# Kernel optimization log

Hardware: AMD Instinct MI355X
Metric: run time of the kernel (lower is better)

Reference implementation:

```python
import jax, jax.numpy as jnp
import numpy as np

GAMMA = 0.99
GAE_LAMBDA = 0.95
SEQ_LEN = 1024
BATCH = 32768


def setup_inputs() -> dict:
    key = jax.random.key(0)
    k1, k2 = jax.random.split(key)
    rewards = jax.random.normal(k1, (SEQ_LEN, BATCH), dtype=jnp.float32)
    values = jax.random.normal(k2, (SEQ_LEN, BATCH), dtype=jnp.float32)
    return {"rewards": rewards, "values": values}


def _compute_advantages(rewards, values, gamma, gae_lambda):
    # delta_t = r_t + gamma * V_{t+1} - V_t  for t = 0 .. T-2  -> [T-1, B]
    deltas = rewards[:-1] + gamma * values[1:] - values[:-1]
    gl = gamma * gae_lambda

    def step(carry, delta):
        adv = delta + gl * carry
        return adv, adv

    init = jnp.zeros_like(deltas[0])
    # reverse scan implements the backward-in-time GAE recurrence
    _, advantages = jax.lax.scan(step, init, deltas, reverse=True)
    return advantages  # [T-1, B], equals torch advantages[:-1]


def reference(rewards, values):
    return _compute_advantages(rewards, values, GAMMA, GAE_LAMBDA)
```

## Files before the change

kernel.cpp:

```cpp
#include <hip/hip_runtime.h>
#include <math.h>


#define T_OUT 1023
#define B2    16384
#define NW    16
#define S_CH  64

#define GAMMA_F 0.99f
#define GL_F    0.9405f
#define INVG_F  1.0632642212653909f

typedef float f2v __attribute__((ext_vector_type(2)));

static __device__ __forceinline__ void nt_store_f2(float2* dst, float2 v) {
  __builtin_nontemporal_store(*(const f2v*)&v, (f2v*)dst);
}

#define STEP2(r, v)                                  \
  p.x = (r).x + GAMMA_F * vn.x - (v).x + GL_F * p.x; \
  p.y = (r).y + GAMMA_F * vn.y - (v).y + GL_F * p.y;

#define P1_LOADQ(rB_, vB_, tt)                       \
  _Pragma("unroll")                                  \
  for (int k = 0; k < 4; ++k) {                      \
    rB_[k] = rp[((tt) - k) * B2];                    \
    vB_[k] = vp[((tt) - k) * B2];                    \
  }

#define P1_COMPQ(rB_, vB_, tt)                       \
  _Pragma("unroll")                                  \
  for (int k = 0; k < 4; ++k) {                      \
    STEP2(rB_[k], vB_[k])                            \
    op[((tt) - k) * B2] = p;                         \
    vn = vB_[k];                                     \
  }

#define P1_BODY(rP, vP, rQ, vQ, rX, vX, rY, vY)      \
  P1_LOADQ(rP, vP, tp)                               \
  P1_LOADQ(rQ, vQ, tp - 4)                           \
  __builtin_amdgcn_sched_barrier(0);                 \
  P1_COMPQ(rX, vX, tc)                               \
  P1_COMPQ(rY, vY, tc - 4)                           \
  tc -= 8; tp -= 8;

#define P1_EPI(rX, vX, rY, vY)                       \
  P1_COMPQ(rX, vX, tc)                               \
  P1_COMPQ(rY, vY, tc - 4)

#define P3_LOADQ(oB_, uu)                            \
  _Pragma("unroll")                                  \
  for (int k = 0; k < 4; ++k) oB_[k] = op[((uu) + k) * B2];

#define P3_COMPQ(oB_, uu)                            \
  _Pragma("unroll")                                  \
  for (int k = 0; k < 4; ++k) {                      \
    oB_[k].x += x.x; oB_[k].y += x.y;                \
    nt_store_f2(&op[((uu) + k) * B2], oB_[k]);       \
    x.x *= INVG_F; x.y *= INVG_F;                    \
  }

#define P3_BODY(oP, oQ, oX, oY)                      \
  P3_LOADQ(oP, up)                                   \
  P3_LOADQ(oQ, up + 4)                               \
  __builtin_amdgcn_sched_barrier(0);                 \
  P3_COMPQ(oX, uc)                                   \
  P3_COMPQ(oY, uc + 4)                               \
  uc += 8; up += 8;

#define P3_EPI(oX, oY)                               \
  P3_COMPQ(oX, uc)                                   \
  P3_COMPQ(oY, uc + 4)

__global__ __launch_bounds__(1024, 4) void gae_fused(
    const float2* __restrict__ r2, const float2* __restrict__ v2,
    float2* __restrict__ o2, float gS_full, float gS_last) {
  __shared__ float2 aggs[NW][64];

  const int lane = threadIdx.x & 63;
  const int w    = threadIdx.x >> 6;
  const int q    = blockIdx.x * 64 + lane;

  const int t_lo = w * S_CH;
  const int t_hi = (w == NW - 1) ? (T_OUT - 1) : (t_lo + S_CH - 1);

  const float2* rp = r2 + q;
  const float2* vp = v2 + q;
  float2*       op = o2 + q;

  float2 vn = vp[(t_hi + 1) * B2];
  float2 p  = make_float2(0.f, 0.f);

  int t = t_hi;
  if (w == NW - 1) {
    float2 rr[7], vv[7];
#pragma unroll
    for (int k = 0; k < 7; ++k) { rr[k] = rp[(t - k) * B2]; vv[k] = vp[(t - k) * B2]; }
#pragma unroll
    for (int k = 0; k < 7; ++k) {
      STEP2(rr[k], vv[k])
      op[(t - k) * B2] = p;
      vn = vv[k];
    }
    t -= 7;
  }

  {
    float2 rA[4], vA[4], rB[4], vB[4], rC[4], vC[4], rD[4], vD[4];
    int tc = t;
    int tp = t - 8;

    P1_LOADQ(rA, vA, tc)
    P1_LOADQ(rB, vB, tc - 4)

    const int nb = ((t - t_lo + 1) >> 3) - 1;
    int i = 0;
    for (; i + 2 <= nb; i += 2) {
      P1_BODY(rC, vC, rD, vD, rA, vA, rB, vB)
      P1_BODY(rA, vA, rB, vB, rC, vC, rD, vD)
    }
    if (i < nb) {
      P1_BODY(rC, vC, rD, vD, rA, vA, rB, vB)
      P1_EPI(rC, vC, rD, vD)
    } else {
      P1_EPI(rA, vA, rB, vB)
    }
  }

  aggs[w][lane] = p;
  __syncthreads();

  float2 K = make_float2(0.f, 0.f);
  for (int j = NW - 1; j > w; --j) {
    const float gj = (j == NW - 1) ? gS_last : gS_full;
    float2 a = aggs[j][lane];
    K.x = a.x + gj * K.x;
    K.y = a.y + gj * K.y;
  }

  if (w < NW - 1) {
    float2 x = make_float2(gS_full * K.x, gS_full * K.y);
    float2 oA[4], oB[4], oC[4], oD[4];
    int uc = t_lo;
    int up = t_lo + 8;

    P3_LOADQ(oA, uc)
    P3_LOADQ(oB, uc + 4)

#pragma unroll 1
    for (int i = 0; i < 3; ++i) {
      P3_BODY(oC, oD, oA, oB)
      P3_BODY(oA, oB, oC, oD)
    }
    P3_BODY(oC, oD, oA, oB)
    P3_EPI(oC, oD)
  }
}

extern "C" void kernel_launch(void* const* d_in, const int* in_sizes, int n_in,
                              void* d_out, int out_size, void* d_ws, size_t ws_size,
                              hipStream_t stream) {
  const float2* r2 = (const float2*)d_in[0];
  const float2* v2 = (const float2*)d_in[1];
  float2* o2 = (float2*)d_out;

  const double g = (double)GL_F;
  const float gS_full = (float)pow(g, S_CH);
  const float gS_last = (float)pow(g, S_CH - 1);

  gae_fused<<<dim3(B2 / 64), dim3(1024), 0, stream>>>(r2, v2, o2, gS_full, gS_last);
}
```

Measured before the change: 348.4 us.

## Split time chunks across blocks with cooperative grid sync

Each block now handles one time chunk for 1024 columns, where before it handled all sixteen chunks for 64 columns. The kernel is launched cooperatively with 256 blocks. Chunk carries are exchanged through global memory after a grid-wide sync, and a second grid sync guards the fix-up pass. The aim is to change the memory access pattern and parallel decomposition. In exchange it pays for two grid barriers and reads carries from global memory instead of shared memory.

```diff
diff --git a/kernel.cpp b/kernel.cpp
--- a/kernel.cpp
+++ b/kernel.cpp
@@ -1,10 +1,12 @@
 #include <hip/hip_runtime.h>
+#include <hip/hip_cooperative_groups.h>
 #include <math.h>
 
 
 #define T_OUT 1023
 #define B2    16384
 #define NW    16
+#define NT_C  16
 #define S_CH  64
 
 #define GAMMA_F 0.99f
@@ -40,13 +42,13 @@
   P1_LOADQ(rP, vP, tp)                               \
   P1_LOADQ(rQ, vQ, tp - 4)                           \
   __builtin_amdgcn_sched_barrier(0);                 \
-  P1_COMPQ(rX, vX, tc)                               \
-  P1_COMPQ(rY, vY, tc - 4)                           \
-  tc -= 8; tp -= 8;
+  P1_COMPQ(rX, vX, tcur)                             \
+  P1_COMPQ(rY, vY, tcur - 4)                         \
+  tcur -= 8; tp -= 8;
 
 #define P1_EPI(rX, vX, rY, vY)                       \
-  P1_COMPQ(rX, vX, tc)                               \
-  P1_COMPQ(rY, vY, tc - 4)
+  P1_COMPQ(rX, vX, tcur)                             \
+  P1_COMPQ(rY, vY, tcur - 4)
 
 #define P3_LOADQ(oB_, uu)                            \
   _Pragma("unroll")                                  \
@@ -75,14 +77,14 @@
 __global__ __launch_bounds__(1024, 4) void gae_fused(
     const float2* __restrict__ r2, const float2* __restrict__ v2,
     float2* __restrict__ o2, float gS_full, float gS_last) {
-  __shared__ float2 aggs[NW][64];
-
   const int lane = threadIdx.x & 63;
   const int w    = threadIdx.x >> 6;
-  const int q    = blockIdx.x * 64 + lane;
+  const int cg   = blockIdx.x & 15;
+  const int tcnk = blockIdx.x >> 4;
 
-  const int t_lo = w * S_CH;
-  const int t_hi = (w == NW - 1) ? (T_OUT - 1) : (t_lo + S_CH - 1);
+  const int q    = cg * 1024 + w * 64 + lane;
+  const int t_lo = tcnk * S_CH;
+  const int t_hi = (tcnk == NT_C - 1) ? (T_OUT - 1) : (t_lo + S_CH - 1);
 
   const float2* rp = r2 + q;
   const float2* vp = v2 + q;
@@ -92,7 +94,7 @@
   float2 p  = make_float2(0.f, 0.f);
 
   int t = t_hi;
-  if (w == NW - 1) {
+  if (tcnk == NT_C - 1) {
     float2 rr[7], vv[7];
 #pragma unroll
     for (int k = 0; k < 7; ++k) { rr[k] = rp[(t - k) * B2]; vv[k] = vp[(t - k) * B2]; }
@@ -107,11 +109,11 @@
 
   {
     float2 rA[4], vA[4], rB[4], vB[4], rC[4], vC[4], rD[4], vD[4];
-    int tc = t;
-    int tp = t - 8;
+    int tcur = t;
+    int tp   = t - 8;
 
-    P1_LOADQ(rA, vA, tc)
-    P1_LOADQ(rB, vB, tc - 4)
+    P1_LOADQ(rA, vA, tcur)
+    P1_LOADQ(rB, vB, tcur - 4)
 
     const int nb = ((t - t_lo + 1) >> 3) - 1;
     int i = 0;
@@ -127,18 +129,19 @@
     }
   }
 
-  aggs[w][lane] = p;
-  __syncthreads();
+  cooperative_groups::this_grid().sync();
 
   float2 K = make_float2(0.f, 0.f);
-  for (int j = NW - 1; j > w; --j) {
-    const float gj = (j == NW - 1) ? gS_last : gS_full;
-    float2 a = aggs[j][lane];
+  for (int j = NT_C - 1; j > tcnk; --j) {
+    const float gj = (j == NT_C - 1) ? gS_last : gS_full;
+    float2 a = op[(j * S_CH) * B2];
     K.x = a.x + gj * K.x;
     K.y = a.y + gj * K.y;
   }
 
-  if (w < NW - 1) {
+  cooperative_groups::this_grid().sync();
+
+  if (tcnk < NT_C - 1) {
     float2 x = make_float2(gS_full * K.x, gS_full * K.y);
     float2 oA[4], oB[4], oC[4], oD[4];
     int uc = t_lo;
@@ -165,8 +168,10 @@
   float2* o2 = (float2*)d_out;
 
   const double g = (double)GL_F;
-  const float gS_full = (float)pow(g, S_CH);
-  const float gS_last = (float)pow(g, S_CH - 1);
+  float gS_full = (float)pow(g, S_CH);
+  float gS_last = (float)pow(g, S_CH - 1);
 
-  gae_fused<<<dim3(B2 / 64), dim3(1024), 0, stream>>>(r2, v2, o2, gS_full, gS_last);
+  void* args[] = {(void*)&r2, (void*)&v2, (void*)&o2, (void*)&gS_full, (void*)&gS_last};
+  hipLaunchCooperativeKernel((const void*)gae_fused, dim3(NT_C * 16), dim3(1024),
+                             args, 0, stream);
 }
```

Result: slower. 471.7 us (+35.4%).

## Keep the last 32 chunk partials in registers to skip the write and re-read

Applied to the files above, without the earlier changes.

Each wave's first 32 recurrence steps (the latest timesteps) are now held in a register array instead of being written to global memory. After the cross-wave carry is known, these values are corrected and stored once, and only the remaining 32 timesteps per chunk are read back and fixed up. The software-pipelined load depth drops from 8 timesteps to 4, and a scalar pre-loop handles leftover steps. This removes part of the global store-then-reload traffic, at the cost of many more registers per thread under a tight launch bound, which risks spills or lower occupancy.

```diff
diff --git a/kernel.cpp b/kernel.cpp
--- a/kernel.cpp
+++ b/kernel.cpp
@@ -36,17 +36,13 @@
     vn = vB_[k];                                     \
   }
 
-#define P1_BODY(rP, vP, rQ, vQ, rX, vX, rY, vY)      \
+#define P1_BODY(rP, vP, rX, vX)                      \
   P1_LOADQ(rP, vP, tp)                               \
-  P1_LOADQ(rQ, vQ, tp - 4)                           \
   __builtin_amdgcn_sched_barrier(0);                 \
-  P1_COMPQ(rX, vX, tc)                               \
-  P1_COMPQ(rY, vY, tc - 4)                           \
-  tc -= 8; tp -= 8;
+  P1_COMPQ(rX, vX, tcur)                             \
+  tcur -= 4; tp -= 4;
 
-#define P1_EPI(rX, vX, rY, vY)                       \
-  P1_COMPQ(rX, vX, tc)                               \
-  P1_COMPQ(rY, vY, tc - 4)
+#define P1_EPI(rX, vX) P1_COMPQ(rX, vX, tcur)
 
 #define P3_LOADQ(oB_, uu)                            \
   _Pragma("unroll")                                  \
@@ -60,17 +56,13 @@
     x.x *= INVG_F; x.y *= INVG_F;                    \
   }
 
-#define P3_BODY(oP, oQ, oX, oY)                      \
-  P3_LOADQ(oP, up)                                   \
-  P3_LOADQ(oQ, up + 4)                               \
+#define P3_BODY(oP, oX)                              \
+  P3_LOADQ(oP, up2)                                  \
   __builtin_amdgcn_sched_barrier(0);                 \
   P3_COMPQ(oX, uc)                                   \
-  P3_COMPQ(oY, uc + 4)                               \
-  uc += 8; up += 8;
+  uc += 4; up2 += 4;
 
-#define P3_EPI(oX, oY)                               \
-  P3_COMPQ(oX, uc)                                   \
-  P3_COMPQ(oY, uc + 4)
+#define P3_EPI(oX) P3_COMPQ(oX, uc)
 
 __global__ __launch_bounds__(1024, 4) void gae_fused(
     const float2* __restrict__ r2, const float2* __restrict__ v2,
@@ -90,40 +82,50 @@
 
   float2 vn = vp[(t_hi + 1) * B2];
   float2 p  = make_float2(0.f, 0.f);
+  float2 psv[32];
 
-  int t = t_hi;
-  if (w == NW - 1) {
-    float2 rr[7], vv[7];
 #pragma unroll
-    for (int k = 0; k < 7; ++k) { rr[k] = rp[(t - k) * B2]; vv[k] = vp[(t - k) * B2]; }
+  for (int j = 0; j < 8; ++j) {
+    float2 rq[4], vq[4];
 #pragma unroll
-    for (int k = 0; k < 7; ++k) {
-      STEP2(rr[k], vv[k])
-      op[(t - k) * B2] = p;
-      vn = vv[k];
+    for (int k = 0; k < 4; ++k) {
+      rq[k] = rp[(t_hi - (j * 4 + k)) * B2];
+      vq[k] = vp[(t_hi - (j * 4 + k)) * B2];
     }
-    t -= 7;
+#pragma unroll
+    for (int k = 0; k < 4; ++k) {
+      STEP2(rq[k], vq[k])
+      psv[j * 4 + k] = p;
+      vn = vq[k];
+    }
   }
 
+  int t = t_hi - 32;
+  const int pre = (t - t_lo + 1) & 3;
+  for (int k = 0; k < pre; ++k, --t) {
+    float2 r = rp[t * B2];
+    float2 v = vp[t * B2];
+    STEP2(r, v)
+    op[t * B2] = p;
+    vn = v;
+  }
   {
-    float2 rA[4], vA[4], rB[4], vB[4], rC[4], vC[4], rD[4], vD[4];
-    int tc = t;
-    int tp = t - 8;
+    float2 rA[4], vA[4], rB[4], vB[4];
+    int tcur = t;
+    int tp   = t - 4;
 
-    P1_LOADQ(rA, vA, tc)
-    P1_LOADQ(rB, vB, tc - 4)
-
-    const int nb = ((t - t_lo + 1) >> 3) - 1;
+    P1_LOADQ(rA, vA, tcur)
+    const int nb = ((t - t_lo + 1) >> 2) - 1;
     int i = 0;
     for (; i + 2 <= nb; i += 2) {
-      P1_BODY(rC, vC, rD, vD, rA, vA, rB, vB)
-      P1_BODY(rA, vA, rB, vB, rC, vC, rD, vD)
+      P1_BODY(rB, vB, rA, vA)
+      P1_BODY(rA, vA, rB, vB)
     }
     if (i < nb) {
-      P1_BODY(rC, vC, rD, vD, rA, vA, rB, vB)
-      P1_EPI(rC, vC, rD, vD)
+      P1_BODY(rB, vB, rA, vA)
+      P1_EPI(rB, vB)
     } else {
-      P1_EPI(rA, vA, rB, vB)
+      P1_EPI(rA, vA)
     }
   }
 
@@ -140,20 +142,32 @@
 
   if (w < NW - 1) {
     float2 x = make_float2(gS_full * K.x, gS_full * K.y);
-    float2 oA[4], oB[4], oC[4], oD[4];
-    int uc = t_lo;
-    int up = t_lo + 8;
+    float2 oA[4], oB[4];
+    int uc  = t_lo;
+    int up2 = t_lo + 4;
 
     P3_LOADQ(oA, uc)
-    P3_LOADQ(oB, uc + 4)
+    P3_BODY(oB, oA)
+    P3_BODY(oA, oB)
+    P3_BODY(oB, oA)
+    P3_BODY(oA, oB)
+    P3_BODY(oB, oA)
+    P3_BODY(oA, oB)
+    P3_BODY(oB, oA)
+    P3_EPI(oB)
+  }
 
-#pragma unroll 1
-    for (int i = 0; i < 3; ++i) {
-      P3_BODY(oC, oD, oA, oB)
-      P3_BODY(oA, oB, oC, oD)
+  {
+    float2 x = make_float2(GL_F * K.x, GL_F * K.y);
+#pragma unroll
+    for (int j = 0; j < 32; ++j) {
+      float2 o;
+      o.x = psv[j].x + x.x;
+      o.y = psv[j].y + x.y;
+      nt_store_f2(&op[(t_hi - j) * B2], o);
+      x.x *= GL_F;
+      x.y *= GL_F;
     }
-    P3_BODY(oC, oD, oA, oB)
-    P3_EPI(oC, oD)
   }
 }
 
```

Measured after the change: 329.7 us. 5.4% less time.
